# Performance work log

Hardware: AMD Instinct MI355X
Metric: run time of the kernel (lower is better)

## Reference

```python
import jax, jax.numpy as jnp
import numpy as np


def make_blur():
    # 5x5x5 separable binomial kernel, normalized to sum 1 then scaled by 8
    k = np.asarray([1, 4, 6, 4, 1], dtype=np.float32)
    k3 = k[:, None, None] * k[None, :, None] * k[None, None, :]
    k3 = k3 / k3.sum() * 8.0
    return jnp.asarray(k3.reshape(1, 1, 5, 5, 5))


def setup_inputs() -> dict:
    key = jax.random.key(0)
    N, C, D, H, W = 2, 32, 48, 48, 48
    x = jax.random.normal(key, (N, C, D, H, W), dtype=jnp.float32)
    return {
        "x": x,
        "blur": make_blur(),
        "output_shape": (N, C, 2 * D, 2 * H, 2 * W),
    }


def reference(x, blur, output_shape):
    N, C, D, H, W = x.shape
    # torch: output_padding[i] = output_shape[i+2] - ((x.shape[i+2]-1)*2 + 1)
    op = tuple(int(output_shape[i + 2]) - ((x.shape[i + 2] - 1) * 2 + 1) for i in range(3))
    pad = blur.shape[-1] // 4  # = 1
    # depthwise: fold channels into batch, single-channel conv
    xr = x.reshape(N * C, 1, D, H, W)
    # replicate pad by 1 on each spatial side (torch F.pad mode='replicate')
    xr = jnp.pad(xr, ((0, 0), (0, 0), (pad, pad), (pad, pad), (pad, pad)), mode='edge')
    # conv_transpose3d(stride=2, padding=4*pad=4, output_padding=op) is equivalent to a
    # conv with lhs_dilation=2 and per-dim padding (k-1-4, k-1-4+op) = (0, op),
    # using the spatially flipped kernel (the binomial kernel is symmetric anyway).
    kern = blur[:, :, ::-1, ::-1, ::-1]
    y = jax.lax.conv_general_dilated(
        xr, kern,
        window_strides=(1, 1, 1),
        padding=[(0, op[0]), (0, op[1]), (0, op[2])],
        lhs_dilation=(2, 2, 2),
        dimension_numbers=('NCDHW', 'OIDHW', 'NCDHW'))
    return y.reshape(N, C, int(output_shape[2]), int(output_shape[3]), int(output_shape[4]))
```

## Files before the change

### kernel.cpp

```cpp
#include <hip/hip_runtime.h>


constexpr int DIN = 48, HIN = 48, WIN = 48;
constexpr int DOUT = 96, HOUT = 96, WOUT = 96;
constexpr int NC = 2 * 32;
constexpr int TPW = WIN / 2;
constexpr int TOTAL = NC * DIN * HIN * TPW;

__global__ __launch_bounds__(256) void Upsample2x2x2_kernel(
    const float* __restrict__ x, float* __restrict__ out)
{
    int idx = blockIdx.x * 256 + threadIdx.x;
    if (idx >= TOTAL) return;

    int t    = idx % TPW;
    int rest = idx / TPW;
    int b    = rest % HIN;
    rest    /= HIN;
    int a    = rest % DIN;
    int nc   = rest / DIN;

    const float* __restrict__ xb = x + (size_t)nc * (DIN * HIN * WIN);

    const int ai[3] = { max(a - 1, 0), a, min(a + 1, DIN - 1) };
    const int bi[3] = { max(b - 1, 0), b, min(b + 1, HIN - 1) };
    const int c0 = 2 * t;
    const int cm = max(c0 - 1, 0);
    const int cp = min(c0 + 2, WIN - 1);

    float r[3][3][4];
    #pragma unroll
    for (int i = 0; i < 3; i++) {
        #pragma unroll
        for (int j = 0; j < 3; j++) {
            const float* __restrict__ row = xb + ((size_t)ai[i] * HIN + bi[j]) * WIN;
            float v0 = row[cm];
            float v1 = row[c0];
            float v2 = row[c0 + 1];
            float v3 = row[cp];
            r[i][j][0] = (v0 + 6.0f * v1 + v2) * 0.125f;
            r[i][j][1] = (v1 + v2) * 0.5f;
            r[i][j][2] = (v1 + 6.0f * v2 + v3) * 0.125f;
            r[i][j][3] = (v2 + v3) * 0.5f;
        }
    }

    float he[3][4], ho[3][4];
    #pragma unroll
    for (int i = 0; i < 3; i++) {
        #pragma unroll
        for (int k = 0; k < 4; k++) {
            he[i][k] = (r[i][0][k] + 6.0f * r[i][1][k] + r[i][2][k]) * 0.125f;
            ho[i][k] = (r[i][1][k] + r[i][2][k]) * 0.5f;
        }
    }

    float o00[4], o01[4], o10[4], o11[4];
    #pragma unroll
    for (int k = 0; k < 4; k++) {
        o00[k] = (he[0][k] + 6.0f * he[1][k] + he[2][k]) * 0.125f;
        o01[k] = (ho[0][k] + 6.0f * ho[1][k] + ho[2][k]) * 0.125f;
        o10[k] = (he[1][k] + he[2][k]) * 0.5f;
        o11[k] = (ho[1][k] + ho[2][k]) * 0.5f;
    }

    float* __restrict__ ob = out + (size_t)nc * (DOUT * HOUT * WOUT);
    size_t base = ((size_t)(2 * a) * HOUT + 2 * b) * WOUT + 4 * t;

    *reinterpret_cast<float4*>(ob + base) =
        make_float4(o00[0], o00[1], o00[2], o00[3]);
    *reinterpret_cast<float4*>(ob + base + WOUT) =
        make_float4(o01[0], o01[1], o01[2], o01[3]);
    *reinterpret_cast<float4*>(ob + base + (size_t)HOUT * WOUT) =
        make_float4(o10[0], o10[1], o10[2], o10[3]);
    *reinterpret_cast<float4*>(ob + base + (size_t)HOUT * WOUT + WOUT) =
        make_float4(o11[0], o11[1], o11[2], o11[3]);
}

extern "C" void kernel_launch(void* const* d_in, const int* in_sizes, int n_in,
                              void* d_out, int out_size, void* d_ws, size_t ws_size,
                              hipStream_t stream) {
    const float* x = (const float*)d_in[0];
    float* out = (float*)d_out;
    int blocks = (TOTAL + 255) / 256;
    Upsample2x2x2_kernel<<<blocks, 256, 0, stream>>>(x, out);
}
```

Before: 57.88 us.

## Compute 2x2 input block per thread with nontemporal stores and folded scaling

Each thread now handles a 2x2 block of input (d,h) positions instead of one, loading a 4x4 neighborhood of rows and reusing the W-filtered values across four output groups. Normalization factors are folded into a single final multiply per output, FMAs replace the separate adds, the center pair is loaded as a float2, and stores use nontemporal hints. This cuts redundant input loads and arithmetic per output. The cost is higher register pressure and a quarter as many threads.

```diff
diff --git a/kernel.cpp b/kernel.cpp
--- a/kernel.cpp
+++ b/kernel.cpp
@@ -1,80 +1,92 @@
 #include <hip/hip_runtime.h>
 
 
+typedef float f32x4 __attribute__((ext_vector_type(4)));
+
 constexpr int DIN = 48, HIN = 48, WIN = 48;
+constexpr int HW = HIN * WIN;
 constexpr int DOUT = 96, HOUT = 96, WOUT = 96;
-constexpr int NC = 2 * 32;
-constexpr int TPW = WIN / 2;
-constexpr int TOTAL = NC * DIN * HIN * TPW;
+constexpr int NC = 64;
+constexpr int THREADS = NC * 24 * 24 * 24;
 
 __global__ __launch_bounds__(256) void Upsample2x2x2_kernel(
     const float* __restrict__ x, float* __restrict__ out)
 {
     int idx = blockIdx.x * 256 + threadIdx.x;
-    if (idx >= TOTAL) return;
+    int t   = idx % 24;
+    int tmp = idx / 24;
+    int b0h = tmp % 24;
+    tmp    /= 24;
+    int a0h = tmp % 24;
+    int nc  = tmp / 24;
 
-    int t    = idx % TPW;
-    int rest = idx / TPW;
-    int b    = rest % HIN;
-    rest    /= HIN;
-    int a    = rest % DIN;
-    int nc   = rest / DIN;
+    const int a0 = a0h * 2, b0 = b0h * 2, w0 = t * 2;
+    const float* __restrict__ xb = x + (size_t)nc * (DIN * HW);
 
-    const float* __restrict__ xb = x + (size_t)nc * (DIN * HIN * WIN);
+    const int ai[4] = { a0 > 0 ? a0 - 1 : 0, a0, a0 + 1,
+                        a0 + 2 < DIN ? a0 + 2 : DIN - 1 };
+    const int bi[4] = { b0 > 0 ? b0 - 1 : 0, b0, b0 + 1,
+                        b0 + 2 < HIN ? b0 + 2 : HIN - 1 };
+    const int wm = w0 > 0 ? w0 - 1 : 0;
+    const int wp = w0 + 2 < WIN ? w0 + 2 : WIN - 1;
 
-    const int ai[3] = { max(a - 1, 0), a, min(a + 1, DIN - 1) };
-    const int bi[3] = { max(b - 1, 0), b, min(b + 1, HIN - 1) };
-    const int c0 = 2 * t;
-    const int cm = max(c0 - 1, 0);
-    const int cp = min(c0 + 2, WIN - 1);
-
-    float r[3][3][4];
+    float r[4][4][4];
     #pragma unroll
-    for (int i = 0; i < 3; i++) {
+    for (int i = 0; i < 4; i++) {
+        const float* __restrict__ xd = xb + ai[i] * HW;
         #pragma unroll
-        for (int j = 0; j < 3; j++) {
-            const float* __restrict__ row = xb + ((size_t)ai[i] * HIN + bi[j]) * WIN;
-            float v0 = row[cm];
-            float v1 = row[c0];
-            float v2 = row[c0 + 1];
-            float v3 = row[cp];
-            r[i][j][0] = (v0 + 6.0f * v1 + v2) * 0.125f;
-            r[i][j][1] = (v1 + v2) * 0.5f;
-            r[i][j][2] = (v1 + 6.0f * v2 + v3) * 0.125f;
-            r[i][j][3] = (v2 + v3) * 0.5f;
+        for (int j = 0; j < 4; j++) {
+            const float* __restrict__ row = xd + bi[j] * WIN;
+            float2 m = *reinterpret_cast<const float2*>(row + w0);
+            float u0 = row[wm];
+            float u3 = row[wp];
+            float u1 = m.x, u2 = m.y;
+            r[i][j][0] = fmaf(6.f, u1, u0) + u2;
+            r[i][j][1] = u1 + u2;
+            r[i][j][2] = fmaf(6.f, u2, u1) + u3;
+            r[i][j][3] = u2 + u3;
         }
     }
 
-    float he[3][4], ho[3][4];
+    float* __restrict__ ob = out + (size_t)nc * (DOUT * HOUT * WOUT);
+    const size_t obase = ((size_t)(a0 * 2) * HOUT + (b0 * 2)) * WOUT + t * 4;
+
     #pragma unroll
-    for (int i = 0; i < 3; i++) {
+    for (int win = 0; win < 2; win++) {
+        float He[4][4], Ho[4][4];
         #pragma unroll
-        for (int k = 0; k < 4; k++) {
-            he[i][k] = (r[i][0][k] + 6.0f * r[i][1][k] + r[i][2][k]) * 0.125f;
-            ho[i][k] = (r[i][1][k] + r[i][2][k]) * 0.5f;
+        for (int i = 0; i < 4; i++)
+            #pragma unroll
+            for (int k = 0; k < 4; k++) {
+                He[i][k] = fmaf(6.f, r[i][win + 1][k], r[i][win][k]) + r[i][win + 2][k];
+                Ho[i][k] = r[i][win + 1][k] + r[i][win + 2][k];
+            }
+
+        #pragma unroll
+        for (int ap = 0; ap < 2; ap++) {
+            float vee[4], voe[4], veo[4], voo[4];
+            #pragma unroll
+            for (int k = 0; k < 4; k++) {
+                vee[k] = fmaf(6.f, He[ap + 1][k], He[ap][k]) + He[ap + 2][k];
+                voe[k] = He[ap + 1][k] + He[ap + 2][k];
+                veo[k] = fmaf(6.f, Ho[ap + 1][k], Ho[ap][k]) + Ho[ap + 2][k];
+                voo[k] = Ho[ap + 1][k] + Ho[ap + 2][k];
+            }
+            size_t rbase = obase + ((size_t)(ap * 2) * HOUT + win * 2) * WOUT;
+            f32x4 s0 = { vee[0] * (1.f/512), vee[1] * (1.f/128),
+                         vee[2] * (1.f/512), vee[3] * (1.f/128) };
+            f32x4 s1 = { veo[0] * (1.f/128), veo[1] * (1.f/32),
+                         veo[2] * (1.f/128), veo[3] * (1.f/32) };
+            f32x4 s2 = { voe[0] * (1.f/128), voe[1] * (1.f/32),
+                         voe[2] * (1.f/128), voe[3] * (1.f/32) };
+            f32x4 s3 = { voo[0] * (1.f/32),  voo[1] * (1.f/8),
+                         voo[2] * (1.f/32),  voo[3] * (1.f/8) };
+            __builtin_nontemporal_store(s0, reinterpret_cast<f32x4*>(ob + rbase));
+            __builtin_nontemporal_store(s1, reinterpret_cast<f32x4*>(ob + rbase + WOUT));
+            __builtin_nontemporal_store(s2, reinterpret_cast<f32x4*>(ob + rbase + (size_t)HOUT * WOUT));
+            __builtin_nontemporal_store(s3, reinterpret_cast<f32x4*>(ob + rbase + (size_t)HOUT * WOUT + WOUT));
         }
     }
-
-    float o00[4], o01[4], o10[4], o11[4];
-    #pragma unroll
-    for (int k = 0; k < 4; k++) {
-        o00[k] = (he[0][k] + 6.0f * he[1][k] + he[2][k]) * 0.125f;
-        o01[k] = (ho[0][k] + 6.0f * ho[1][k] + ho[2][k]) * 0.125f;
-        o10[k] = (he[1][k] + he[2][k]) * 0.5f;
-        o11[k] = (ho[1][k] + ho[2][k]) * 0.5f;
-    }
-
-    float* __restrict__ ob = out + (size_t)nc * (DOUT * HOUT * WOUT);
-    size_t base = ((size_t)(2 * a) * HOUT + 2 * b) * WOUT + 4 * t;
-
-    *reinterpret_cast<float4*>(ob + base) =
-        make_float4(o00[0], o00[1], o00[2], o00[3]);
-    *reinterpret_cast<float4*>(ob + base + WOUT) =
-        make_float4(o01[0], o01[1], o01[2], o01[3]);
-    *reinterpret_cast<float4*>(ob + base + (size_t)HOUT * WOUT) =
-        make_float4(o10[0], o10[1], o10[2], o10[3]);
-    *reinterpret_cast<float4*>(ob + base + (size_t)HOUT * WOUT + WOUT) =
-        make_float4(o11[0], o11[1], o11[2], o11[3]);
 }
 
 extern "C" void kernel_launch(void* const* d_in, const int* in_sizes, int n_in,
@@ -82,6 +94,6 @@
                               hipStream_t stream) {
     const float* x = (const float*)d_in[0];
     float* out = (float*)d_out;
-    int blocks = (TOTAL + 255) / 256;
+    int blocks = THREADS / 256;
     Upsample2x2x2_kernel<<<blocks, 256, 0, stream>>>(x, out);
 }
```

Result: faster. 47.79 us (-17.4%).

## Remap threads to one H output row each, use vector loads and nontemporal stores

Applied to the files above, without the earlier changes.

Each thread now produces the two depth-adjacent float4 outputs for a single output H row instead of a 2x2 block, which doubles the thread count. It uses a 3D grid to drop the integer div/mod index math and replaces the four scalar loads per input row with one 16-byte vector load that is shifted at the edges. The arithmetic is refactored into FMAs with a single final scale, and the stores become nontemporal so the large output write stream is not meant to pollute cache. In exchange, input rows are reloaded by more threads, and the unaligned 16-byte loads may cost more.

```diff
diff --git a/kernel.cpp b/kernel.cpp
--- a/kernel.cpp
+++ b/kernel.cpp
@@ -1,80 +1,82 @@
 #include <hip/hip_runtime.h>
 
 
+typedef float f32x4 __attribute__((ext_vector_type(4)));
+
 constexpr int DIN = 48, HIN = 48, WIN = 48;
-constexpr int DOUT = 96, HOUT = 96, WOUT = 96;
-constexpr int NC = 2 * 32;
-constexpr int TPW = WIN / 2;
-constexpr int TOTAL = NC * DIN * HIN * TPW;
+constexpr int HW = HIN * WIN;
+constexpr int PS = 96 * 96;
 
 __global__ __launch_bounds__(256) void Upsample2x2x2_kernel(
     const float* __restrict__ x, float* __restrict__ out)
 {
-    int idx = blockIdx.x * 256 + threadIdx.x;
-    if (idx >= TOTAL) return;
+    const int p  = blockIdx.x * 256 + threadIdx.x;
+    const int a  = blockIdx.y;
+    const int nc = blockIdx.z;
 
-    int t    = idx % TPW;
-    int rest = idx / TPW;
-    int b    = rest % HIN;
-    rest    /= HIN;
-    int a    = rest % DIN;
-    int nc   = rest / DIN;
+    const int h    = p / 24;
+    const int s    = p - h * 24;
+    const int b    = h >> 1;
+    const int hodd = h & 1;
 
-    const float* __restrict__ xb = x + (size_t)nc * (DIN * HIN * WIN);
+    const float* __restrict__ xb = x + nc * (DIN * HW);
 
-    const int ai[3] = { max(a - 1, 0), a, min(a + 1, DIN - 1) };
-    const int bi[3] = { max(b - 1, 0), b, min(b + 1, HIN - 1) };
-    const int c0 = 2 * t;
-    const int cm = max(c0 - 1, 0);
-    const int cp = min(c0 + 2, WIN - 1);
+    const int ii[3] = { a > 0 ? a - 1 : 0, a, a + 1 < DIN ? a + 1 : DIN - 1 };
 
-    float r[3][3][4];
+    const int jb1 = b + 1 < HIN ? b + 1 : HIN - 1;
+    const int jj[3] = { hodd ? b : (b > 0 ? b - 1 : 0),
+                        hodd ? jb1 : b,
+                        jb1 };
+    const float hw[3] = { hodd ? 4.f : 1.f, hodd ? 4.f : 6.f, hodd ? 0.f : 1.f };
+
+    const bool lo = (s == 0), hi = (s == 23);
+    const int base = 2 * s + (lo ? 0 : (hi ? -2 : -1));
+
+    float hc[3][4];
     #pragma unroll
     for (int i = 0; i < 3; i++) {
+        const float* __restrict__ xd = xb + ii[i] * HW;
+        float a0 = 0.f, a1 = 0.f, a2 = 0.f, a3 = 0.f;
         #pragma unroll
         for (int j = 0; j < 3; j++) {
-            const float* __restrict__ row = xb + ((size_t)ai[i] * HIN + bi[j]) * WIN;
-            float v0 = row[cm];
-            float v1 = row[c0];
-            float v2 = row[c0 + 1];
-            float v3 = row[cp];
-            r[i][j][0] = (v0 + 6.0f * v1 + v2) * 0.125f;
-            r[i][j][1] = (v1 + v2) * 0.5f;
-            r[i][j][2] = (v1 + 6.0f * v2 + v3) * 0.125f;
-            r[i][j][3] = (v2 + v3) * 0.5f;
+            const float* __restrict__ row = xd + jj[j] * WIN;
+            f32x4 v;
+            __builtin_memcpy(&v, row + base, 16);
+            float u0 = hi ? v.y : v.x;
+            float u1 = lo ? v.x : (hi ? v.z : v.y);
+            float u2 = lo ? v.y : (hi ? v.w : v.z);
+            float u3 = lo ? v.z : v.w;
+            float w = hw[j];
+            a0 = fmaf(w, u0, a0);
+            a1 = fmaf(w, u1, a1);
+            a2 = fmaf(w, u2, a2);
+            a3 = fmaf(w, u3, a3);
         }
+        hc[i][0] = a0; hc[i][1] = a1; hc[i][2] = a2; hc[i][3] = a3;
     }
 
-    float he[3][4], ho[3][4];
+    float Wv[3][4];
     #pragma unroll
     for (int i = 0; i < 3; i++) {
-        #pragma unroll
-        for (int k = 0; k < 4; k++) {
-            he[i][k] = (r[i][0][k] + 6.0f * r[i][1][k] + r[i][2][k]) * 0.125f;
-            ho[i][k] = (r[i][1][k] + r[i][2][k]) * 0.5f;
-        }
+        Wv[i][0] = fmaf(6.f, hc[i][1], hc[i][0]) + hc[i][2];
+        Wv[i][1] = (hc[i][1] + hc[i][2]) * 4.f;
+        Wv[i][2] = fmaf(6.f, hc[i][2], hc[i][1]) + hc[i][3];
+        Wv[i][3] = (hc[i][2] + hc[i][3]) * 4.f;
     }
 
-    float o00[4], o01[4], o10[4], o11[4];
-    #pragma unroll
-    for (int k = 0; k < 4; k++) {
-        o00[k] = (he[0][k] + 6.0f * he[1][k] + he[2][k]) * 0.125f;
-        o01[k] = (ho[0][k] + 6.0f * ho[1][k] + ho[2][k]) * 0.125f;
-        o10[k] = (he[1][k] + he[2][k]) * 0.5f;
-        o11[k] = (ho[1][k] + ho[2][k]) * 0.5f;
-    }
+    f32x4 e, o;
+    e.x = (fmaf(6.f, Wv[1][0], Wv[0][0]) + Wv[2][0]) * (1.f/512);
+    e.y = (fmaf(6.f, Wv[1][1], Wv[0][1]) + Wv[2][1]) * (1.f/512);
+    e.z = (fmaf(6.f, Wv[1][2], Wv[0][2]) + Wv[2][2]) * (1.f/512);
+    e.w = (fmaf(6.f, Wv[1][3], Wv[0][3]) + Wv[2][3]) * (1.f/512);
+    o.x = (Wv[1][0] + Wv[2][0]) * (4.f/512);
+    o.y = (Wv[1][1] + Wv[2][1]) * (4.f/512);
+    o.z = (Wv[1][2] + Wv[2][2]) * (4.f/512);
+    o.w = (Wv[1][3] + Wv[2][3]) * (4.f/512);
 
-    float* __restrict__ ob = out + (size_t)nc * (DOUT * HOUT * WOUT);
-    size_t base = ((size_t)(2 * a) * HOUT + 2 * b) * WOUT + 4 * t;
-
-    *reinterpret_cast<float4*>(ob + base) =
-        make_float4(o00[0], o00[1], o00[2], o00[3]);
-    *reinterpret_cast<float4*>(ob + base + WOUT) =
-        make_float4(o01[0], o01[1], o01[2], o01[3]);
-    *reinterpret_cast<float4*>(ob + base + (size_t)HOUT * WOUT) =
-        make_float4(o10[0], o10[1], o10[2], o10[3]);
-    *reinterpret_cast<float4*>(ob + base + (size_t)HOUT * WOUT + WOUT) =
-        make_float4(o11[0], o11[1], o11[2], o11[3]);
+    float* __restrict__ ob = out + (nc * 96 + 2 * a) * PS;
+    __builtin_nontemporal_store(e, reinterpret_cast<f32x4*>(ob + p * 4));
+    __builtin_nontemporal_store(o, reinterpret_cast<f32x4*>(ob + PS + p * 4));
 }
 
 extern "C" void kernel_launch(void* const* d_in, const int* in_sizes, int n_in,
@@ -82,6 +84,6 @@
                               hipStream_t stream) {
     const float* x = (const float*)d_in[0];
     float* out = (float*)d_out;
-    int blocks = (TOTAL + 255) / 256;
-    Upsample2x2x2_kernel<<<blocks, 256, 0, stream>>>(x, out);
+    dim3 grid(9, 48, 64);
+    Upsample2x2x2_kernel<<<grid, 256, 0, stream>>>(x, out);
 }
```

Result: faster. 50.87 us (-12.1%).
